# Optimization experiments

Hardware: AMD Instinct MI355X
Metric: run time of the kernel (lower is better)

Reference implementation:

```python
import jax, jax.numpy as jnp
import numpy as np

T = 8192
C = 768
HEAD = 64

def setup_inputs() -> dict:
    key = jax.random.key(0)
    k0, k1, k2, k3 = jax.random.split(key, 4)
    tokens = jax.random.normal(k0, (T, C), dtype=jnp.float32)
    Wk = jax.random.normal(k1, (C, HEAD), dtype=jnp.float32) * (1.0 / np.sqrt(C))
    Wq = jax.random.normal(k2, (C, HEAD), dtype=jnp.float32) * (1.0 / np.sqrt(C))
    Wv = jax.random.normal(k3, (C, HEAD), dtype=jnp.float32) * (1.0 / np.sqrt(C))
    return {"tokens": tokens, "Wk": Wk, "Wq": Wq, "Wv": Wv}

def reference(tokens, Wk, Wq, Wv):
    # Single-head causal attention, faithful to source (scale = C**0.5, a multiply).
    keys = tokens @ Wk          # [T, H]
    queries = tokens @ Wq       # [T, H]
    values = tokens @ Wv        # [T, H]
    c = tokens.shape[-1]
    wei = (queries @ keys.T) * (c ** 0.5)                 # [T, T]
    causal = jnp.tril(jnp.ones((tokens.shape[0], tokens.shape[0]), dtype=bool))
    wei = jnp.where(causal, wei, -jnp.inf)
    wei = jax.nn.softmax(wei, axis=-1)
    return wei @ values         # [T, H]; dropout inactive (training=False)
```

## Files before the change

kernel.cpp:

```cpp
#include <hip/hip_runtime.h>
#include <math.h>

#define T_TOK 8192
#define C_DIM 768
#define H_DIM 64
#define SCALE_LOG2E (27.712812921102035f * 1.4426950408889634f)
#define NSPLIT 4

typedef _Float16 half8 __attribute__((ext_vector_type(8)));
typedef float floatx4 __attribute__((ext_vector_type(4)));

#define MFMA16(a, b, c) __builtin_amdgcn_mfma_f32_16x16x32_f16(a, b, c, 0, 0, 0)
#define WAIT_LGKM0() __builtin_amdgcn_s_waitcnt(0xC07F)
#define EXP2F(x) __builtin_amdgcn_exp2f(x)


__global__ __launch_bounds__(64) void wconvert_kernel(
    const float* __restrict__ Wk, const float* __restrict__ Wq,
    const float* __restrict__ Wv, _Float16* __restrict__ WF)
{
    const int b = blockIdx.x;
    const int mat = b / 96, rem = b % 96, kt = rem >> 2, nb = rem & 3;
    const int lane = threadIdx.x & 63, l15 = lane & 15, quad = lane >> 4;
    const float* __restrict__ W = (mat == 0) ? Wk : (mat == 1) ? Wq : Wv;

    half8 h, l;
#pragma unroll
    for (int j = 0; j < 8; ++j) {
        const float v = W[(kt * 32 + quad * 8 + j) * H_DIM + nb * 16 + l15];
        const _Float16 hv = (_Float16)v;
        h[j] = hv;
        l[j] = (_Float16)(v - (float)hv);
    }
    _Float16* dst = WF + ((((size_t)mat * 24 + kt) * 4 + nb) * 2) * 512 + lane * 8;
    *(half8*)dst = h;
    *(half8*)(dst + 512) = l;
}

__global__ __launch_bounds__(64) void proj_kernel(
    const float* __restrict__ tokens, const _Float16* __restrict__ WF,
    _Float16* __restrict__ KF, _Float16* __restrict__ QF,
    _Float16* __restrict__ VF)
{
    __shared__ float Cb[32 * 68];
    const int b = blockIdx.x;
    const int mat = b >> 8, mi = b & 255;
    const int lane = threadIdx.x & 63, l15 = lane & 15, quad = lane >> 4;
    const int row0 = mi * 32;

    floatx4 acc[2][4];
#pragma unroll
    for (int mb = 0; mb < 2; ++mb)
#pragma unroll
        for (int nb = 0; nb < 4; ++nb) acc[mb][nb] = 0;

    const _Float16* __restrict__ wfm = WF + (size_t)mat * 24 * 4 * 2 * 512;
    const float* __restrict__ xb0 = tokens + (size_t)(row0 + l15) * C_DIM + quad * 8;
    const float* __restrict__ xb1 = tokens + (size_t)(row0 + 16 + l15) * C_DIM + quad * 8;

    float4 tf[4][4];
#pragma unroll
    for (int d = 0; d < 4; ++d) {
        tf[d][0] = *(const float4*)(xb0 + d * 32);
        tf[d][1] = *(const float4*)(xb0 + d * 32 + 4);
        tf[d][2] = *(const float4*)(xb1 + d * 32);
        tf[d][3] = *(const float4*)(xb1 + d * 32 + 4);
    }
    half8 nwh[4], nwl[4];
#pragma unroll
    for (int nb = 0; nb < 4; ++nb) {
        const _Float16* wp = wfm + ((size_t)nb * 2) * 512 + lane * 8;
        nwh[nb] = *(const half8*)wp;
        nwl[nb] = (mat != 2) ? *(const half8*)(wp + 512) : nwh[nb];
    }

#pragma unroll
    for (int kt = 0; kt < 24; ++kt) {
        const int slot = kt & 3;
        const float4 x0 = tf[slot][0], x1 = tf[slot][1];
        const float4 x2 = tf[slot][2], x3 = tf[slot][3];
        half8 wh[4], wl[4];
#pragma unroll
        for (int nb = 0; nb < 4; ++nb) { wh[nb] = nwh[nb]; wl[nb] = nwl[nb]; }

        const int ktn = (kt < 23) ? kt + 1 : 23;
#pragma unroll
        for (int nb = 0; nb < 4; ++nb) {
            const _Float16* wp = wfm + (((size_t)ktn * 4 + nb) * 2) * 512 + lane * 8;
            nwh[nb] = *(const half8*)wp;
            nwl[nb] = (mat != 2) ? *(const half8*)(wp + 512) : nwh[nb];
        }
        if (kt + 4 < 24) {
            const int ktf = kt + 4;
            tf[slot][0] = *(const float4*)(xb0 + ktf * 32);
            tf[slot][1] = *(const float4*)(xb0 + ktf * 32 + 4);
            tf[slot][2] = *(const float4*)(xb1 + ktf * 32);
            tf[slot][3] = *(const float4*)(xb1 + ktf * 32 + 4);
        }

        half8 ah[2], al[2];
        {
            const float xs0[8] = {x0.x, x0.y, x0.z, x0.w, x1.x, x1.y, x1.z, x1.w};
            const float xs1[8] = {x2.x, x2.y, x2.z, x2.w, x3.x, x3.y, x3.z, x3.w};
#pragma unroll
            for (int e = 0; e < 8; ++e) {
                _Float16 hv = (_Float16)xs0[e];
                ah[0][e] = hv;
                al[0][e] = (_Float16)(xs0[e] - (float)hv);
                hv = (_Float16)xs1[e];
                ah[1][e] = hv;
                al[1][e] = (_Float16)(xs1[e] - (float)hv);
            }
        }

#pragma unroll
        for (int nb = 0; nb < 4; ++nb) {
            if (mat != 2) {
#pragma unroll
                for (int mb = 0; mb < 2; ++mb) {
                    acc[mb][nb] = MFMA16(ah[mb], wh[nb], acc[mb][nb]);
                    acc[mb][nb] = MFMA16(ah[mb], wl[nb], acc[mb][nb]);
                    acc[mb][nb] = MFMA16(al[mb], wh[nb], acc[mb][nb]);
                }
            } else {
#pragma unroll
                for (int mb = 0; mb < 2; ++mb)
                    acc[mb][nb] = MFMA16(ah[mb], wh[nb], acc[mb][nb]);
            }
        }
    }

#pragma unroll
    for (int mb = 0; mb < 2; ++mb)
#pragma unroll
        for (int nb = 0; nb < 4; ++nb)
#pragma unroll
            for (int r = 0; r < 4; ++r)
                Cb[(mb * 16 + quad * 4 + r) * 68 + nb * 16 + l15] = acc[mb][nb][r];
    __builtin_amdgcn_wave_barrier();
    WAIT_LGKM0();
    __builtin_amdgcn_wave_barrier();

    if (mat != 2) {
#pragma unroll
        for (int nbL = 0; nbL < 2; ++nbL) {
#pragma unroll
            for (int ks = 0; ks < 2; ++ks) {
                const float* cp = Cb + (nbL * 16 + l15) * 68 + ks * 32 + quad * 8;
                const float4 c0 = *(const float4*)cp;
                const float4 c1 = *(const float4*)(cp + 4);
                const float cs[8] = {c0.x, c0.y, c0.z, c0.w, c1.x, c1.y, c1.z, c1.w};
                half8 h, l;
#pragma unroll
                for (int e = 0; e < 8; ++e) {
                    const _Float16 hv = (_Float16)cs[e];
                    h[e] = hv;
                    l[e] = (_Float16)(cs[e] - (float)hv);
                }
                _Float16* dst;
                if (mat == 0) {
                    const int t = mi >> 1, nb = (mi & 1) * 2 + nbL;
                    dst = KF + (((size_t)(t * 4 + nb) * 2 + ks) * 2) * 512 + lane * 8;
                } else {
                    const int rb = mi * 2 + nbL;
                    dst = QF + (((size_t)rb * 2 + ks) * 2) * 512 + lane * 8;
                }
                *(half8*)dst = h;
                *(half8*)(dst + 512) = l;
            }
        }
    } else {
        const int t = mi >> 1, ks = mi & 1;
#pragma unroll
        for (int nb = 0; nb < 4; ++nb) {
            half8 h;
#pragma unroll
            for (int j = 0; j < 8; ++j)
                h[j] = (_Float16)Cb[(quad * 8 + j) * 68 + nb * 16 + l15];
            *(half8*)(VF + ((size_t)(t * 4 + nb) * 2 + ks) * 512 + lane * 8) = h;
        }
    }
}

__global__ __launch_bounds__(512, 2) void attn_mfma_kernel(
    const _Float16* __restrict__ QF, const _Float16* __restrict__ KF,
    const _Float16* __restrict__ VF,
    float* __restrict__ pm, float* __restrict__ pl, float* __restrict__ po)
{
    __shared__ __align__(16) float smemf[9216];
    _Float16* Ps = (_Float16*)smemf;

    const int w = threadIdx.x >> 6, lane = threadIdx.x & 63;
    const int l15 = lane & 15, quad = lane >> 4;
    const int mhalf = w & 1, ss = w >> 1;

    const int b = blockIdx.x;
    const int j = b & 255, hb = b >> 8;
    const int qt = (hb == 0) ? (j >> 1) : (127 - (j >> 1));
    const int sp = (hb << 1) | (j & 1);

    const int qbase = qt * 64;
    const int wrow0 = qbase + mhalf * 32;

    half8 qh[2][2], ql[2][2];
#pragma unroll
    for (int mb = 0; mb < 2; ++mb)
#pragma unroll
        for (int ks = 0; ks < 2; ++ks) {
            const int rb = qt * 4 + mhalf * 2 + mb;
            const _Float16* qp = QF + (((size_t)rb * 2 + ks) * 2) * 512 + lane * 8;
            qh[mb][ks] = *(const half8*)qp;
            ql[mb][ks] = *(const half8*)(qp + 512);
        }

    floatx4 O[2][4];
#pragma unroll
    for (int mb = 0; mb < 2; ++mb)
#pragma unroll
        for (int nb = 0; nb < 4; ++nb) O[mb][nb] = 0;
    float mreg[2][4], lreg[2][4];
#pragma unroll
    for (int mb = 0; mb < 2; ++mb)
#pragma unroll
        for (int r = 0; r < 4; ++r) { mreg[mb][r] = -INFINITY; lreg[mb][r] = 0.f; }

    const int t0 = sp + 4 * ss;
    half8 bh[4][2], bl[4][2];
    if (t0 <= qt) {
#pragma unroll
        for (int nb = 0; nb < 4; ++nb)
#pragma unroll
            for (int ks = 0; ks < 2; ++ks) {
                const _Float16* kp =
                    KF + (((size_t)(t0 * 4 + nb) * 2 + ks) * 2) * 512 + lane * 8;
                bh[nb][ks] = *(const half8*)kp;
                bl[nb][ks] = *(const half8*)(kp + 512);
            }
    }

    for (int t = t0; t <= qt; t += 16) {
        const int kb = t * 64;

        half8 v0r[4], v1r[4];
#pragma unroll
        for (int nb = 0; nb < 4; ++nb) {
            const _Float16* vp = VF + ((size_t)(t * 4 + nb) * 2) * 512 + lane * 8;
            v0r[nb] = *(const half8*)vp;
            v1r[nb] = *(const half8*)(vp + 512);
        }

        float sv[2][4][4];
#pragma unroll
        for (int mb = 0; mb < 2; ++mb)
#pragma unroll
            for (int nb = 0; nb < 4; ++nb) {
                floatx4 s = 0;
#pragma unroll
                for (int ks = 0; ks < 2; ++ks) {
                    s = MFMA16(qh[mb][ks], bh[nb][ks], s);
                    s = MFMA16(qh[mb][ks], bl[nb][ks], s);
                    s = MFMA16(ql[mb][ks], bh[nb][ks], s);
                }
#pragma unroll
                for (int r = 0; r < 4; ++r) sv[mb][nb][r] = s[r] * SCALE_LOG2E;
            }

        if (t + 16 <= qt) {
            const int tn = t + 16;
#pragma unroll
            for (int nb = 0; nb < 4; ++nb)
#pragma unroll
                for (int ks = 0; ks < 2; ++ks) {
                    const _Float16* kp =
                        KF + (((size_t)(tn * 4 + nb) * 2 + ks) * 2) * 512 + lane * 8;
                    bh[nb][ks] = *(const half8*)kp;
                    bl[nb][ks] = *(const half8*)(kp + 512);
                }
        }

        if (kb + 63 > wrow0) {
#pragma unroll
            for (int mb = 0; mb < 2; ++mb) {
                const int rowbase = wrow0 + mb * 16 + quad * 4;
#pragma unroll
                for (int nb = 0; nb < 4; ++nb) {
                    const int col = kb + nb * 16 + l15;
#pragma unroll
                    for (int r = 0; r < 4; ++r)
                        if (col > rowbase + r) sv[mb][nb][r] = -INFINITY;
                }
            }
        }

#pragma unroll
        for (int mb = 0; mb < 2; ++mb) {
#pragma unroll
            for (int r = 0; r < 4; ++r) {
                float rm = fmaxf(fmaxf(sv[mb][0][r], sv[mb][1][r]),
                                 fmaxf(sv[mb][2][r], sv[mb][3][r]));
                rm = fmaxf(rm, __shfl_xor(rm, 1));
                rm = fmaxf(rm, __shfl_xor(rm, 2));
                rm = fmaxf(rm, __shfl_xor(rm, 4));
                rm = fmaxf(rm, __shfl_xor(rm, 8));
                const float mnew = fmaxf(mreg[mb][r], rm);
                const float alpha = EXP2F(mreg[mb][r] - mnew);
                float psum = 0.f;
#pragma unroll
                for (int nb = 0; nb < 4; ++nb) {
                    const float p = EXP2F(sv[mb][nb][r] - mnew);
                    psum += p;
                    Ps[(w * 2 + mb) * 1152 + (quad * 4 + r) * 72 + nb * 16 + l15] =
                        (_Float16)p;
                }
                lreg[mb][r] = lreg[mb][r] * alpha + psum;
                mreg[mb][r] = mnew;
#pragma unroll
                for (int nb = 0; nb < 4; ++nb) O[mb][nb][r] *= alpha;
            }
        }

        __builtin_amdgcn_wave_barrier();
        WAIT_LGKM0();
        __builtin_amdgcn_wave_barrier();
        half8 pa0[2], pa1[2];
#pragma unroll
        for (int mb = 0; mb < 2; ++mb) {
            const _Float16* pp = Ps + (w * 2 + mb) * 1152 + l15 * 72 + quad * 8;
            pa0[mb] = *(const half8*)pp;
            pa1[mb] = *(const half8*)(pp + 32);
        }

#pragma unroll
        for (int nb = 0; nb < 4; ++nb) {
#pragma unroll
            for (int mb = 0; mb < 2; ++mb) {
                O[mb][nb] = MFMA16(pa0[mb], v0r[nb], O[mb][nb]);
                O[mb][nb] = MFMA16(pa1[mb], v1r[nb], O[mb][nb]);
            }
        }
        __builtin_amdgcn_wave_barrier();
    }

#pragma unroll
    for (int mb = 0; mb < 2; ++mb)
#pragma unroll
        for (int r = 0; r < 4; ++r) {
            float s = lreg[mb][r];
            s += __shfl_xor(s, 1);
            s += __shfl_xor(s, 2);
            s += __shfl_xor(s, 4);
            s += __shfl_xor(s, 8);
            lreg[mb][r] = s;
        }

    __syncthreads();
    if (ss >= 2) {
        const int slot = ss - 2;
#pragma unroll
        for (int mb = 0; mb < 2; ++mb)
#pragma unroll
            for (int r = 0; r < 4; ++r) {
                const int row32 = mb * 16 + quad * 4 + r;
                const int sidx = (slot * 2 + mhalf) * 32 + row32;
#pragma unroll
                for (int nb = 0; nb < 4; ++nb)
                    smemf[sidx * 64 + nb * 16 + l15] = O[mb][nb][r];
                if (l15 == 0) {
                    smemf[8192 + sidx] = mreg[mb][r];
                    smemf[8320 + sidx] = lreg[mb][r];
                }
            }
    }
    __syncthreads();
    if (ss < 2) {
        const int slot = ss;
#pragma unroll
        for (int mb = 0; mb < 2; ++mb)
#pragma unroll
            for (int r = 0; r < 4; ++r) {
                const int row32 = mb * 16 + quad * 4 + r;
                const int sidx = (slot * 2 + mhalf) * 32 + row32;
                const float m1 = mreg[mb][r], l1 = lreg[mb][r];
                const float m2 = smemf[8192 + sidx];
                const float l2 = smemf[8320 + sidx];
                const float mm = fmaxf(m1, m2);
                const float a1 = (m1 == -INFINITY) ? 0.f : EXP2F(m1 - mm);
                const float a2 = (m2 == -INFINITY) ? 0.f : EXP2F(m2 - mm);
#pragma unroll
                for (int nb = 0; nb < 4; ++nb)
                    O[mb][nb][r] = O[mb][nb][r] * a1 +
                                   smemf[sidx * 64 + nb * 16 + l15] * a2;
                mreg[mb][r] = mm;
                lreg[mb][r] = l1 * a1 + l2 * a2;
            }
    }
    __syncthreads();
    if (ss == 1) {
#pragma unroll
        for (int mb = 0; mb < 2; ++mb)
#pragma unroll
            for (int r = 0; r < 4; ++r) {
                const int row32 = mb * 16 + quad * 4 + r;
                const int sidx = mhalf * 32 + row32;
#pragma unroll
                for (int nb = 0; nb < 4; ++nb)
                    smemf[sidx * 64 + nb * 16 + l15] = O[mb][nb][r];
                if (l15 == 0) {
                    smemf[8192 + sidx] = mreg[mb][r];
                    smemf[8320 + sidx] = lreg[mb][r];
                }
            }
    }
    __syncthreads();
    if (ss == 0) {
        const int pidx = qt * NSPLIT + sp;
#pragma unroll
        for (int mb = 0; mb < 2; ++mb)
#pragma unroll
            for (int r = 0; r < 4; ++r) {
                const int row32 = mb * 16 + quad * 4 + r;
                const int sidx = mhalf * 32 + row32;
                const float m1 = mreg[mb][r], l1 = lreg[mb][r];
                const float m2 = smemf[8192 + sidx];
                const float l2 = smemf[8320 + sidx];
                const float mm = fmaxf(m1, m2);
                const float a1 = (m1 == -INFINITY) ? 0.f : EXP2F(m1 - mm);
                const float a2 = (m2 == -INFINITY) ? 0.f : EXP2F(m2 - mm);
                const int row = mhalf * 32 + row32;
                float* dst = po + ((size_t)pidx * 64 + row) * 64;
#pragma unroll
                for (int nb = 0; nb < 4; ++nb)
                    dst[nb * 16 + l15] =
                        O[mb][nb][r] * a1 + smemf[sidx * 64 + nb * 16 + l15] * a2;
                if (l15 == 0) {
                    pm[pidx * 64 + row] = mm;
                    pl[pidx * 64 + row] = l1 * a1 + l2 * a2;
                }
            }
    }
}

__global__ __launch_bounds__(256) void combine_kernel(
    const float* __restrict__ pm, const float* __restrict__ pl,
    const float* __restrict__ po, float* __restrict__ out)
{
    const int vid = blockIdx.x * 256 + threadIdx.x;
    const int row = vid >> 4;
    const int d4  = vid & 15;
    const int qt  = row >> 6;
    const int r   = row & 63;

    float mm = -INFINITY;
#pragma unroll
    for (int s = 0; s < NSPLIT; ++s)
        mm = fmaxf(mm, pm[(qt * NSPLIT + s) * 64 + r]);
    float L = 0.f;
    float4 val = make_float4(0.f, 0.f, 0.f, 0.f);
#pragma unroll
    for (int s = 0; s < NSPLIT; ++s) {
        const int p = (qt * NSPLIT + s) * 64 + r;
        const float mp = pm[p];
        const float sc = (mp > -INFINITY) ? EXP2F(mp - mm) : 0.f;
        L += pl[p] * sc;
        const float4 v = *(const float4*)(po + (size_t)p * H_DIM + d4 * 4);
        val.x += v.x * sc; val.y += v.y * sc;
        val.z += v.z * sc; val.w += v.w * sc;
    }
    const float inv = 1.0f / L;
    float4 o; o.x = val.x * inv; o.y = val.y * inv;
    o.z = val.z * inv; o.w = val.w * inv;
    *(float4*)(out + (size_t)row * H_DIM + d4 * 4) = o;
}

extern "C" void kernel_launch(void* const* d_in, const int* in_sizes, int n_in,
                              void* d_out, int out_size, void* d_ws, size_t ws_size,
                              hipStream_t stream)
{
    const float* tokens = (const float*)d_in[0];
    const float* Wk = (const float*)d_in[1];
    const float* Wq = (const float*)d_in[2];
    const float* Wv = (const float*)d_in[3];
    float* out = (float*)d_out;

    char* ws = (char*)d_ws;
    const size_t MB = 1024 * 1024;
    _Float16* WF = (_Float16*)(ws + 0 * MB);
    _Float16* KF = (_Float16*)(ws + 1 * MB);
    _Float16* QF = (_Float16*)(ws + 3 * MB);
    _Float16* VF = (_Float16*)(ws + 5 * MB);
    float* pm = (float*)(ws + 6 * MB);
    float* pl = (float*)(ws + 6 * MB + 128 * 1024);
    float* po = (float*)(ws + 6 * MB + 256 * 1024);

    wconvert_kernel<<<288, 64, 0, stream>>>(Wk, Wq, Wv, WF);

    proj_kernel<<<768, 64, 0, stream>>>(tokens, WF, KF, QF, VF);

    attn_mfma_kernel<<<128 * NSPLIT, 512, 0, stream>>>(QF, KF, VF, pm, pl, po);

    combine_kernel<<<T_TOK * H_DIM / 4 / 256, 256, 0, stream>>>(pm, pl, po, out);
}
```

Baseline: 145.3 us.

## Fuse K/Q/V projections into one block per token tile

Each proj_kernel block now computes all three projections (K, Q, V) for its 32-token tile instead of one matrix per block, so the token tile is loaded from global memory and split into fp16 hi/lo only once rather than three times. The grid drops from 768 to 256 single-wave blocks, with weight prefetch double-buffered per matrix and an LDS staging buffer three times larger. In exchange, the kernel needs far more registers per wave (three accumulator sets plus five weight fragment sets) and there are fewer blocks to spread across CUs.

Measured after the change: 150.7 us. +3.7%, slower.

```diff
diff --git a/kernel.cpp b/kernel.cpp
--- a/kernel.cpp
+++ b/kernel.cpp
@@ -37,24 +37,27 @@
     *(half8*)(dst + 512) = l;
 }
 
-__global__ __launch_bounds__(64) void proj_kernel(
+__global__ __launch_bounds__(64, 1) void proj_kernel(
     const float* __restrict__ tokens, const _Float16* __restrict__ WF,
     _Float16* __restrict__ KF, _Float16* __restrict__ QF,
     _Float16* __restrict__ VF)
 {
-    __shared__ float Cb[32 * 68];
+    __shared__ float Cb[3 * 32 * 68];
     const int b = blockIdx.x;
-    const int mat = b >> 8, mi = b & 255;
     const int lane = threadIdx.x & 63, l15 = lane & 15, quad = lane >> 4;
-    const int row0 = mi * 32;
-
-    floatx4 acc[2][4];
-#pragma unroll
-    for (int mb = 0; mb < 2; ++mb)
-#pragma unroll
-        for (int nb = 0; nb < 4; ++nb) acc[mb][nb] = 0;
-
-    const _Float16* __restrict__ wfm = WF + (size_t)mat * 24 * 4 * 2 * 512;
+    const int row0 = b * 32;
+
+    floatx4 acc[3][2][4];
+#pragma unroll
+    for (int mat = 0; mat < 3; ++mat)
+#pragma unroll
+        for (int mb = 0; mb < 2; ++mb)
+#pragma unroll
+            for (int nb = 0; nb < 4; ++nb) acc[mat][mb][nb] = 0;
+
+    const _Float16* __restrict__ wK = WF + lane * 8;
+    const _Float16* __restrict__ wQ = wK + 24 * 4 * 2 * 512;
+    const _Float16* __restrict__ wV = wQ + 24 * 4 * 2 * 512;
     const float* __restrict__ xb0 = tokens + (size_t)(row0 + l15) * C_DIM + quad * 8;
     const float* __restrict__ xb1 = tokens + (size_t)(row0 + 16 + l15) * C_DIM + quad * 8;
 
@@ -66,29 +69,33 @@
         tf[d][2] = *(const float4*)(xb1 + d * 32);
         tf[d][3] = *(const float4*)(xb1 + d * 32 + 4);
     }
-    half8 nwh[4], nwl[4];
+    half8 wkh[2][4], wkl[2][4], wqh[2][4], wql[2][4], wvh[2][4];
 #pragma unroll
     for (int nb = 0; nb < 4; ++nb) {
-        const _Float16* wp = wfm + ((size_t)nb * 2) * 512 + lane * 8;
-        nwh[nb] = *(const half8*)wp;
-        nwl[nb] = (mat != 2) ? *(const half8*)(wp + 512) : nwh[nb];
+        wkh[0][nb] = *(const half8*)(wK + (size_t)(nb * 2) * 512);
+        wkl[0][nb] = *(const half8*)(wK + (size_t)(nb * 2 + 1) * 512);
+        wqh[0][nb] = *(const half8*)(wQ + (size_t)(nb * 2) * 512);
+        wql[0][nb] = *(const half8*)(wQ + (size_t)(nb * 2 + 1) * 512);
+        wvh[0][nb] = *(const half8*)(wV + (size_t)(nb * 2) * 512);
     }
 
 #pragma unroll
     for (int kt = 0; kt < 24; ++kt) {
         const int slot = kt & 3;
+        const int cur = kt & 1, nxt = cur ^ 1;
         const float4 x0 = tf[slot][0], x1 = tf[slot][1];
         const float4 x2 = tf[slot][2], x3 = tf[slot][3];
-        half8 wh[4], wl[4];
-#pragma unroll
-        for (int nb = 0; nb < 4; ++nb) { wh[nb] = nwh[nb]; wl[nb] = nwl[nb]; }
-
-        const int ktn = (kt < 23) ? kt + 1 : 23;
-#pragma unroll
-        for (int nb = 0; nb < 4; ++nb) {
-            const _Float16* wp = wfm + (((size_t)ktn * 4 + nb) * 2) * 512 + lane * 8;
-            nwh[nb] = *(const half8*)wp;
-            nwl[nb] = (mat != 2) ? *(const half8*)(wp + 512) : nwh[nb];
+
+        if (kt < 23) {
+            const int ktn = kt + 1;
+#pragma unroll
+            for (int nb = 0; nb < 4; ++nb) {
+                wkh[nxt][nb] = *(const half8*)(wK + (size_t)((ktn * 4 + nb) * 2) * 512);
+                wkl[nxt][nb] = *(const half8*)(wK + (size_t)((ktn * 4 + nb) * 2 + 1) * 512);
+                wqh[nxt][nb] = *(const half8*)(wQ + (size_t)((ktn * 4 + nb) * 2) * 512);
+                wql[nxt][nb] = *(const half8*)(wQ + (size_t)((ktn * 4 + nb) * 2 + 1) * 512);
+                wvh[nxt][nb] = *(const half8*)(wV + (size_t)((ktn * 4 + nb) * 2) * 512);
+            }
         }
         if (kt + 4 < 24) {
             const int ktf = kt + 4;
@@ -115,37 +122,38 @@
 
 #pragma unroll
         for (int nb = 0; nb < 4; ++nb) {
-            if (mat != 2) {
-#pragma unroll
-                for (int mb = 0; mb < 2; ++mb) {
-                    acc[mb][nb] = MFMA16(ah[mb], wh[nb], acc[mb][nb]);
-                    acc[mb][nb] = MFMA16(ah[mb], wl[nb], acc[mb][nb]);
-                    acc[mb][nb] = MFMA16(al[mb], wh[nb], acc[mb][nb]);
-                }
-            } else {
-#pragma unroll
-                for (int mb = 0; mb < 2; ++mb)
-                    acc[mb][nb] = MFMA16(ah[mb], wh[nb], acc[mb][nb]);
-            }
-        }
-    }
-
-#pragma unroll
-    for (int mb = 0; mb < 2; ++mb)
-#pragma unroll
-        for (int nb = 0; nb < 4; ++nb)
-#pragma unroll
-            for (int r = 0; r < 4; ++r)
-                Cb[(mb * 16 + quad * 4 + r) * 68 + nb * 16 + l15] = acc[mb][nb][r];
+#pragma unroll
+            for (int mb = 0; mb < 2; ++mb) {
+                acc[0][mb][nb] = MFMA16(ah[mb], wkh[cur][nb], acc[0][mb][nb]);
+                acc[0][mb][nb] = MFMA16(ah[mb], wkl[cur][nb], acc[0][mb][nb]);
+                acc[0][mb][nb] = MFMA16(al[mb], wkh[cur][nb], acc[0][mb][nb]);
+                acc[1][mb][nb] = MFMA16(ah[mb], wqh[cur][nb], acc[1][mb][nb]);
+                acc[1][mb][nb] = MFMA16(ah[mb], wql[cur][nb], acc[1][mb][nb]);
+                acc[1][mb][nb] = MFMA16(al[mb], wqh[cur][nb], acc[1][mb][nb]);
+                acc[2][mb][nb] = MFMA16(ah[mb], wvh[cur][nb], acc[2][mb][nb]);
+            }
+        }
+    }
+
+#pragma unroll
+    for (int mat = 0; mat < 3; ++mat)
+#pragma unroll
+        for (int mb = 0; mb < 2; ++mb)
+#pragma unroll
+            for (int nb = 0; nb < 4; ++nb)
+#pragma unroll
+                for (int r = 0; r < 4; ++r)
+                    Cb[mat * 2176 + (mb * 16 + quad * 4 + r) * 68 + nb * 16 + l15] =
+                        acc[mat][mb][nb][r];
     __builtin_amdgcn_wave_barrier();
     WAIT_LGKM0();
     __builtin_amdgcn_wave_barrier();
 
-    if (mat != 2) {
-#pragma unroll
-        for (int nbL = 0; nbL < 2; ++nbL) {
-#pragma unroll
-            for (int ks = 0; ks < 2; ++ks) {
+#pragma unroll
+    for (int nbL = 0; nbL < 2; ++nbL) {
+#pragma unroll
+        for (int ks = 0; ks < 2; ++ks) {
+            {
                 const float* cp = Cb + (nbL * 16 + l15) * 68 + ks * 32 + quad * 8;
                 const float4 c0 = *(const float4*)cp;
                 const float4 c1 = *(const float4*)(cp + 4);
@@ -157,26 +165,41 @@
                     h[e] = hv;
                     l[e] = (_Float16)(cs[e] - (float)hv);
                 }
-                _Float16* dst;
-                if (mat == 0) {
-                    const int t = mi >> 1, nb = (mi & 1) * 2 + nbL;
-                    dst = KF + (((size_t)(t * 4 + nb) * 2 + ks) * 2) * 512 + lane * 8;
-                } else {
-                    const int rb = mi * 2 + nbL;
-                    dst = QF + (((size_t)rb * 2 + ks) * 2) * 512 + lane * 8;
-                }
+                const int t = b >> 1, nb = (b & 1) * 2 + nbL;
+                _Float16* dst =
+                    KF + (((size_t)(t * 4 + nb) * 2 + ks) * 2) * 512 + lane * 8;
                 *(half8*)dst = h;
                 *(half8*)(dst + 512) = l;
             }
-        }
-    } else {
-        const int t = mi >> 1, ks = mi & 1;
+            {
+                const float* cp =
+                    Cb + 2176 + (nbL * 16 + l15) * 68 + ks * 32 + quad * 8;
+                const float4 c0 = *(const float4*)cp;
+                const float4 c1 = *(const float4*)(cp + 4);
+                const float cs[8] = {c0.x, c0.y, c0.z, c0.w, c1.x, c1.y, c1.z, c1.w};
+                half8 h, l;
+#pragma unroll
+                for (int e = 0; e < 8; ++e) {
+                    const _Float16 hv = (_Float16)cs[e];
+                    h[e] = hv;
+                    l[e] = (_Float16)(cs[e] - (float)hv);
+                }
+                const int rb = b * 2 + nbL;
+                _Float16* dst = QF + (((size_t)rb * 2 + ks) * 2) * 512 + lane * 8;
+                *(half8*)dst = h;
+                *(half8*)(dst + 512) = l;
+            }
+        }
+    }
+
+    {
+        const int t = b >> 1, ks = b & 1;
 #pragma unroll
         for (int nb = 0; nb < 4; ++nb) {
             half8 h;
 #pragma unroll
             for (int j = 0; j < 8; ++j)
-                h[j] = (_Float16)Cb[(quad * 8 + j) * 68 + nb * 16 + l15];
+                h[j] = (_Float16)Cb[2 * 2176 + (quad * 8 + j) * 68 + nb * 16 + l15];
             *(half8*)(VF + ((size_t)(t * 4 + nb) * 2 + ks) * 512 + lane * 8) = h;
         }
     }
@@ -494,7 +517,7 @@
 
     wconvert_kernel<<<288, 64, 0, stream>>>(Wk, Wq, Wv, WF);
 
-    proj_kernel<<<768, 64, 0, stream>>>(tokens, WF, KF, QF, VF);
+    proj_kernel<<<256, 64, 0, stream>>>(tokens, WF, KF, QF, VF);
 
     attn_mfma_kernel<<<128 * NSPLIT, 512, 0, stream>>>(QF, KF, VF, pm, pl, po);
 
```
